# Optimization experiments

Hardware: AMD Instinct MI355X
Metric: run time of the kernel (lower is better)

## Reference

```python
import jax, jax.numpy as jnp
import numpy as np

POOL_LIST = (1, 2, 4)  # pyramid levels -> 1x1, 2x2, 4x4 bins


def _spp_mix(x, pool_list=POOL_LIST):
    """Spatial pyramid pooling, pool_type='mix' (max + mean), channels_last.

    x: (B, H, W, C) -> (B, sum(p*p for p in pool_list) * C)
    Matches the original TF loop ordering: for each level, outer loop over
    bin columns (jy), inner loop over bin rows (ix).
    """
    B, H, W, C = x.shape
    outs = []
    for p in pool_list:
        wr, wc = H // p, W // p  # window rows/cols (floor div, as in original)
        # crop to covered region, then split into p x p bins in one reshape
        xs = x[:, :p * wr, :p * wc, :].reshape(B, p, wr, p, wc, C)
        # mix = max + mean over each window
        v = xs.max(axis=(2, 4)) + xs.mean(axis=(2, 4))  # (B, pr, pc, C)
        # original appends in (jy outer, ix inner) order -> transpose rows/cols
        v = jnp.transpose(v, (0, 2, 1, 3)).reshape(B, p * p * C)
        outs.append(v)
    return jnp.concatenate(outs, axis=-1)


def setup_inputs() -> dict:
    key = jax.random.key(0)
    x = jax.random.normal(key, (32, 64, 64, 512), dtype=jnp.float32)
    return {"x": x}


def reference(x) -> jnp.ndarray:
    return _spp_mix(x)
```

## Files before the change

kernel.cpp:

```cpp
#include <hip/hip_runtime.h>
#include <math.h>


#define B_ 32
#define HW_ 64
#define C_ 512
#define CVEC 128

__device__ __forceinline__ float4 f4max(float4 a, float4 b) {
    return make_float4(fmaxf(a.x, b.x), fmaxf(a.y, b.y),
                       fmaxf(a.z, b.z), fmaxf(a.w, b.w));
}
__device__ __forceinline__ float4 f4add(float4 a, float4 b) {
    return make_float4(a.x + b.x, a.y + b.y, a.z + b.z, a.w + b.w);
}
__device__ __forceinline__ float4 f4mix(float4 m, float4 s, float inv) {
    return make_float4(m.x + s.x * inv, m.y + s.y * inv,
                       m.z + s.z * inv, m.w + s.w * inv);
}

__global__ __launch_bounds__(256) void spp_bins_kernel(
    const float4* __restrict__ x,
    float4* __restrict__ maxbuf,
    float4* __restrict__ sumbuf)
{
    const int blk  = blockIdx.x;
    const int b    = blk >> 4;
    const int bin  = blk & 15;
    const int br   = bin >> 2;
    const int bc   = bin & 3;
    const int tid  = threadIdx.x;
    const int cg   = tid & (CVEC - 1);
    const int half = tid >> 7;

    const int base = ((b * HW_ + br * 16) * HW_ + bc * 16) * CVEC + cg;

    float4 mx = make_float4(-INFINITY, -INFINITY, -INFINITY, -INFINITY);
    float4 sm = make_float4(0.f, 0.f, 0.f, 0.f);

    #pragma unroll 8
    for (int k = 0; k < 128; ++k) {
        const int s = (half << 7) + k;
        const int i = s >> 4;
        const int j = s & 15;
        const float4 v = x[base + (i * HW_ + j) * CVEC];
        mx = f4max(mx, v);
        sm = f4add(sm, v);
    }

    __shared__ float4 smax[CVEC];
    __shared__ float4 ssum[CVEC];
    if (half == 1) { smax[cg] = mx; ssum[cg] = sm; }
    __syncthreads();
    if (half == 0) {
        mx = f4max(mx, smax[cg]);
        sm = f4add(sm, ssum[cg]);
        const int o = (b * 16 + bin) * CVEC + cg;
        maxbuf[o] = mx;
        sumbuf[o] = sm;
    }
}

__global__ __launch_bounds__(256) void spp_agg_kernel(
    const float4* __restrict__ maxbuf,
    const float4* __restrict__ sumbuf,
    float4* __restrict__ out)
{
    const int idx = blockIdx.x * 256 + threadIdx.x;
    const int b   = idx >> 7;
    const int cg  = idx & (CVEC - 1);

    float4 m[16], s[16];
    #pragma unroll
    for (int bin = 0; bin < 16; ++bin) {
        const int o = (b * 16 + bin) * CVEC + cg;
        m[bin] = maxbuf[o];
        s[bin] = sumbuf[o];
    }

    const int row = b * (21 * CVEC);

    #pragma unroll
    for (int br = 0; br < 4; ++br) {
        #pragma unroll
        for (int bc = 0; bc < 4; ++bc) {
            const int bin = br * 4 + bc;
            out[row + 5 * CVEC + (bc * 4 + br) * CVEC + cg] =
                f4mix(m[bin], s[bin], 1.0f / 256.0f);
        }
    }

    float4 m2[4], s2[4];
    #pragma unroll
    for (int pr = 0; pr < 2; ++pr) {
        #pragma unroll
        for (int pc = 0; pc < 2; ++pc) {
            const int b00 = (2 * pr) * 4 + (2 * pc);
            float4 mm = f4max(f4max(m[b00], m[b00 + 1]),
                              f4max(m[b00 + 4], m[b00 + 5]));
            float4 ss = f4add(f4add(s[b00], s[b00 + 1]),
                              f4add(s[b00 + 4], s[b00 + 5]));
            m2[pr * 2 + pc] = mm;
            s2[pr * 2 + pc] = ss;
            out[row + CVEC + (pc * 2 + pr) * CVEC + cg] =
                f4mix(mm, ss, 1.0f / 1024.0f);
        }
    }

    float4 mm = f4max(f4max(m2[0], m2[1]), f4max(m2[2], m2[3]));
    float4 ss = f4add(f4add(s2[0], s2[1]), f4add(s2[2], s2[3]));
    out[row + cg] = f4mix(mm, ss, 1.0f / 4096.0f);
}

extern "C" void kernel_launch(void* const* d_in, const int* in_sizes, int n_in,
                              void* d_out, int out_size, void* d_ws, size_t ws_size,
                              hipStream_t stream) {
    const float4* x = (const float4*)d_in[0];
    float* ws = (float*)d_ws;
    float4* maxbuf = (float4*)ws;
    float4* sumbuf = (float4*)(ws + B_ * 16 * C_);
    float4* out = (float4*)d_out;

    spp_bins_kernel<<<B_ * 16, 256, 0, stream>>>(x, maxbuf, sumbuf);
    spp_agg_kernel<<<(B_ * CVEC) / 256, 256, 0, stream>>>(maxbuf, sumbuf, out);
}
```

Measured before the change: 352.1 us.

## Fuse bin and aggregation kernels with last-block atomic counter per batch

Merges the two kernels into one. Each block now uses 512 threads split into four row-quarters of a 16x16 bin, writes the 4x4-level output directly, then increments a per-batch atomic counter. The last block for a batch computes the 2x2 and 1x1 levels from the partial buffers. This removes a second kernel launch and its dependency gap, and doubles per-block parallelism, at the cost of atomics, threadfences and a serial tail in one block per batch. Counters depend on atomicInc wraparound and on the workspace being zeroed initially.

```diff
diff --git a/kernel.cpp b/kernel.cpp
--- a/kernel.cpp
+++ b/kernel.cpp
@@ -19,97 +19,89 @@
                        m.z + s.z * inv, m.w + s.w * inv);
 }
 
-__global__ __launch_bounds__(256) void spp_bins_kernel(
+__global__ __launch_bounds__(512) void spp_fused_kernel(
     const float4* __restrict__ x,
     float4* __restrict__ maxbuf,
-    float4* __restrict__ sumbuf)
+    float4* __restrict__ sumbuf,
+    unsigned int* counters,
+    float4* __restrict__ out)
 {
-    const int blk  = blockIdx.x;
-    const int b    = blk >> 4;
-    const int bin  = blk & 15;
-    const int br   = bin >> 2;
-    const int bc   = bin & 3;
-    const int tid  = threadIdx.x;
-    const int cg   = tid & (CVEC - 1);
-    const int half = tid >> 7;
+    const int blk = blockIdx.x;
+    const int b   = blk >> 4;
+    const int bin = blk & 15;
+    const int br  = bin >> 2;
+    const int bc  = bin & 3;
+    const int tid = threadIdx.x;
+    const int cg  = tid & (CVEC - 1);
+    const int q   = tid >> 7;
 
-    const int base = ((b * HW_ + br * 16) * HW_ + bc * 16) * CVEC + cg;
+    const int base = ((b * HW_ + br * 16 + q * 4) * HW_ + bc * 16) * CVEC + cg;
 
     float4 mx = make_float4(-INFINITY, -INFINITY, -INFINITY, -INFINITY);
     float4 sm = make_float4(0.f, 0.f, 0.f, 0.f);
 
     #pragma unroll 8
-    for (int k = 0; k < 128; ++k) {
-        const int s = (half << 7) + k;
-        const int i = s >> 4;
-        const int j = s & 15;
-        const float4 v = x[base + (i * HW_ + j) * CVEC];
+    for (int k = 0; k < 64; ++k) {
+        const int r = k >> 4;
+        const int j = k & 15;
+        const float4 v = x[base + (r * HW_ + j) * CVEC];
         mx = f4max(mx, v);
         sm = f4add(sm, v);
     }
 
-    __shared__ float4 smax[CVEC];
-    __shared__ float4 ssum[CVEC];
-    if (half == 1) { smax[cg] = mx; ssum[cg] = sm; }
+    __shared__ float4 smax[3][CVEC];
+    __shared__ float4 ssum[3][CVEC];
+    __shared__ int lastflag;
+
+    if (q > 0) { smax[q - 1][cg] = mx; ssum[q - 1][cg] = sm; }
     __syncthreads();
-    if (half == 0) {
-        mx = f4max(mx, smax[cg]);
-        sm = f4add(sm, ssum[cg]);
+    if (q == 0) {
+        mx = f4max(f4max(mx, smax[0][cg]), f4max(smax[1][cg], smax[2][cg]));
+        sm = f4add(f4add(sm, ssum[0][cg]), f4add(ssum[1][cg], ssum[2][cg]));
         const int o = (b * 16 + bin) * CVEC + cg;
         maxbuf[o] = mx;
         sumbuf[o] = sm;
+        out[b * (21 * CVEC) + 5 * CVEC + (bc * 4 + br) * CVEC + cg] =
+            f4mix(mx, sm, 1.0f / 256.0f);
+        __threadfence();
     }
-}
+    __syncthreads();
 
-__global__ __launch_bounds__(256) void spp_agg_kernel(
-    const float4* __restrict__ maxbuf,
-    const float4* __restrict__ sumbuf,
-    float4* __restrict__ out)
-{
-    const int idx = blockIdx.x * 256 + threadIdx.x;
-    const int b   = idx >> 7;
-    const int cg  = idx & (CVEC - 1);
+    if (tid == 0) {
+        unsigned int ret = atomicInc(&counters[b * 64], 15u);
+        lastflag = (ret == 14u) ? 1 : 0;
+    }
+    __syncthreads();
 
-    float4 m[16], s[16];
-    #pragma unroll
-    for (int bin = 0; bin < 16; ++bin) {
-        const int o = (b * 16 + bin) * CVEC + cg;
-        m[bin] = maxbuf[o];
-        s[bin] = sumbuf[o];
+    if (lastflag && tid < CVEC) {
+        __threadfence();
+        const int pbase = b * 16 * CVEC + cg;
+        const int row   = b * (21 * CVEC);
+        float4 m1 = make_float4(-INFINITY, -INFINITY, -INFINITY, -INFINITY);
+        float4 s1 = make_float4(0.f, 0.f, 0.f, 0.f);
+        #pragma unroll
+        for (int pr = 0; pr < 2; ++pr) {
+            #pragma unroll
+            for (int pc = 0; pc < 2; ++pc) {
+                float4 mm = make_float4(-INFINITY, -INFINITY, -INFINITY, -INFINITY);
+                float4 ss = make_float4(0.f, 0.f, 0.f, 0.f);
+                #pragma unroll
+                for (int dr = 0; dr < 2; ++dr) {
+                    #pragma unroll
+                    for (int dc = 0; dc < 2; ++dc) {
+                        const int bb = (2 * pr + dr) * 4 + (2 * pc + dc);
+                        mm = f4max(mm, maxbuf[pbase + bb * CVEC]);
+                        ss = f4add(ss, sumbuf[pbase + bb * CVEC]);
+                    }
+                }
+                out[row + CVEC + (pc * 2 + pr) * CVEC + cg] =
+                    f4mix(mm, ss, 1.0f / 1024.0f);
+                m1 = f4max(m1, mm);
+                s1 = f4add(s1, ss);
+            }
+        }
+        out[row + cg] = f4mix(m1, s1, 1.0f / 4096.0f);
     }
-
-    const int row = b * (21 * CVEC);
-
-    #pragma unroll
-    for (int br = 0; br < 4; ++br) {
-        #pragma unroll
-        for (int bc = 0; bc < 4; ++bc) {
-            const int bin = br * 4 + bc;
-            out[row + 5 * CVEC + (bc * 4 + br) * CVEC + cg] =
-                f4mix(m[bin], s[bin], 1.0f / 256.0f);
-        }
-    }
-
-    float4 m2[4], s2[4];
-    #pragma unroll
-    for (int pr = 0; pr < 2; ++pr) {
-        #pragma unroll
-        for (int pc = 0; pc < 2; ++pc) {
-            const int b00 = (2 * pr) * 4 + (2 * pc);
-            float4 mm = f4max(f4max(m[b00], m[b00 + 1]),
-                              f4max(m[b00 + 4], m[b00 + 5]));
-            float4 ss = f4add(f4add(s[b00], s[b00 + 1]),
-                              f4add(s[b00 + 4], s[b00 + 5]));
-            m2[pr * 2 + pc] = mm;
-            s2[pr * 2 + pc] = ss;
-            out[row + CVEC + (pc * 2 + pr) * CVEC + cg] =
-                f4mix(mm, ss, 1.0f / 1024.0f);
-        }
-    }
-
-    float4 mm = f4max(f4max(m2[0], m2[1]), f4max(m2[2], m2[3]));
-    float4 ss = f4add(f4add(s2[0], s2[1]), f4add(s2[2], s2[3]));
-    out[row + cg] = f4mix(mm, ss, 1.0f / 4096.0f);
 }
 
 extern "C" void kernel_launch(void* const* d_in, const int* in_sizes, int n_in,
@@ -119,8 +111,8 @@
     float* ws = (float*)d_ws;
     float4* maxbuf = (float4*)ws;
     float4* sumbuf = (float4*)(ws + B_ * 16 * C_);
+    unsigned int* counters = (unsigned int*)(ws + 2 * B_ * 16 * C_);
     float4* out = (float4*)d_out;
 
-    spp_bins_kernel<<<B_ * 16, 256, 0, stream>>>(x, maxbuf, sumbuf);
-    spp_agg_kernel<<<(B_ * CVEC) / 256, 256, 0, stream>>>(maxbuf, sumbuf, out);
+    spp_fused_kernel<<<B_ * 16, 512, 0, stream>>>(x, maxbuf, sumbuf, counters, out);
 }
```

Measured after the change: 414.6 us. +17.7%, slower.
